# Kernel optimization log

Hardware: AMD Instinct MI355X
Metric: run time of the kernel (lower is better)

The kernel has to match this reference:

```python
import jax, jax.numpy as jnp
import numpy as np
import math

DIM = 256
B, H, W = 8, 64, 64


def setup_inputs() -> dict:
    key = jax.random.key(0)
    ks = jax.random.split(key, 8)
    d4 = DIM // 4
    s = 1.0 / math.sqrt(DIM)
    return {
        "sem": jax.random.normal(ks[0], (B, DIM, H, W), jnp.float32),
        "foren": jax.random.normal(ks[1], (B, DIM, H, W), jnp.float32),
        "Wq": jax.random.normal(ks[2], (d4, DIM), jnp.float32) * s,
        "bq": jnp.zeros((d4,), jnp.float32),
        "Wk": jax.random.normal(ks[3], (d4, DIM), jnp.float32) * s,
        "bk": jnp.zeros((d4,), jnp.float32),
        "Wv": jax.random.normal(ks[4], (DIM, DIM), jnp.float32) * s,
        "bv": jnp.zeros((DIM,), jnp.float32),
        "gamma": jnp.zeros((1,), jnp.float32),
    }


def reference(sem, foren, Wq, bq, Wk, bk, Wv, bv, gamma):
    Bn, C, Hn, Wn = sem.shape
    HW = Hn * Wn
    # 1x1 convs == per-pixel linear projections
    q = jnp.einsum('oc,bchw->bohw', Wq, sem) + bq[None, :, None, None]
    k = jnp.einsum('oc,bchw->bohw', Wk, foren) + bk[None, :, None, None]
    v = jnp.einsum('oc,bchw->bohw', Wv, foren) + bv[None, :, None, None]
    q = q.reshape(Bn, -1, HW).transpose(0, 2, 1)        # [B, HW, C/4]
    k = k.reshape(Bn, -1, HW)                           # [B, C/4, HW]
    v = v.reshape(Bn, C, HW)                            # [B, C, HW]
    attn = jnp.einsum('bnd,bdm->bnm', q, k) / math.sqrt(C // 4)
    attn = jax.nn.softmax(attn, axis=-1)                # [B, HW, HW]
    out = jnp.einsum('bcm,bnm->bcn', v, attn).reshape(Bn, C, Hn, Wn)
    return sem + gamma * out
```

## Files before the change

kernel.cpp:

```cpp
#include <hip/hip_runtime.h>
#include <stdint.h>

typedef unsigned short u16;
typedef unsigned int u32;
typedef short s16x8 __attribute__((ext_vector_type(8)));
typedef float f32x4 __attribute__((ext_vector_type(4)));
typedef float f32x16 __attribute__((ext_vector_type(16)));
typedef u32 u32x2 __attribute__((ext_vector_type(2)));

#define DIM 256
#define HW  4096
#define NB  8
#define QSCL 0.18033688011112042f

template <int N> struct ic { static constexpr int value = N; };

__device__ __forceinline__ u16 f2bf(float f) {
  union { float f; unsigned u; } v; v.f = f;
  unsigned r = v.u + 0x7FFFu + ((v.u >> 16) & 1u);
  return (u16)(r >> 16);
}
__device__ __forceinline__ float fexp2(float x) { return __builtin_amdgcn_exp2f(x); }

typedef __attribute__((address_space(1))) const void gvoid_c;
typedef __attribute__((address_space(3))) void lvoid;
__device__ __forceinline__ void gload_lds16(const void* g, void* l) {
  __builtin_amdgcn_global_load_lds((gvoid_c*)g, (lvoid*)l, 16, 0, 0);
}
__device__ __forceinline__ f32x16 mfma32(s16x8 a, s16x8 b, f32x16 c) {
  return __builtin_amdgcn_mfma_f32_32x32x16_bf16(a, b, c, 0, 0, 0);
}
__device__ __forceinline__ f32x4 mfma16(s16x8 a, s16x8 b, f32x4 c) {
  return __builtin_amdgcn_mfma_f32_16x16x32_bf16(a, b, c, 0, 0, 0);
}

__global__ void prep_w(const float* __restrict__ Wq, const float* __restrict__ Wk,
                       const float* __restrict__ Wv, u16* __restrict__ dst,
                       u32* __restrict__ knmax_u) {
  int idx = blockIdx.x * 256 + threadIdx.x;
  if (blockIdx.x == 0 && threadIdx.x < 8) knmax_u[threadIdx.x] = 0u;
  float v;
  if (idx < 16384)        v = Wq[idx] * QSCL;
  else if (idx < 32768)   v = Wk[idx - 16384];
  else                    v = Wv[idx - 32768];
  dst[idx] = f2bf(v);
}

__global__ __launch_bounds__(256) void proj_all(
    const float* __restrict__ sem, const float* __restrict__ foren,
    const u16* __restrict__ Wqb, const u16* __restrict__ Wkb, const u16* __restrict__ Wvb,
    const float* __restrict__ bq, const float* __restrict__ bk, const float* __restrict__ bv,
    u16* __restrict__ Qo, u16* __restrict__ Ko, u16* __restrict__ Vo,
    float* __restrict__ qnsq, u32* __restrict__ knmax_u) {
  __shared__ u16 lds[16384];
  const bool qpath = blockIdx.x < 512;
  const int bid = qpath ? blockIdx.x : blockIdx.x - 512;
  const int t = threadIdx.x, b = bid & 7, n0 = (bid >> 3) * 64;
  const float* X = qpath ? sem : foren;
  {
    const int px = t & 63, cb = (t >> 6) * 8, swz = (px & 31) * 8;
    for (int i = 0; i < 8; ++i) {
      int c0 = i * 32 + cb;
      size_t gb = ((size_t)b * DIM + c0) * HW + n0 + px;
      s16x8 us;
#pragma unroll
      for (int j = 0; j < 8; ++j) us[j] = (short)f2bf(X[gb + (size_t)j * HW]);
      *(s16x8*)(lds + px * 256 + (c0 ^ swz)) = us;
    }
  }
  __syncthreads();
  const int w = t >> 6, lane = t & 63, l15 = lane & 15, g = lane >> 4;

  if (qpath) {
    const int px = w * 16 + l15;
    s16x8 bx[8];
#pragma unroll
    for (int kc = 0; kc < 8; ++kc)
      bx[kc] = *(const s16x8*)(lds + px * 256 + (((kc * 4 + g) ^ (px & 31)) * 8));
    float nrm = 0.f;
#pragma unroll
    for (int ct = 0; ct < 4; ++ct) {
      f32x4 bb = *(const f32x4*)(bq + ct * 16 + 4 * g);
      f32x4 acc;
#pragma unroll
      for (int j = 0; j < 4; ++j) acc[j] = bb[j] * QSCL;
#pragma unroll
      for (int kc = 0; kc < 8; ++kc) {
        s16x8 aw = *(const s16x8*)(Wqb + (ct * 16 + l15) * 256 + kc * 32 + g * 8);
        acc = mfma16(aw, bx[kc], acc);
      }
      u32 lo = (u32)f2bf(acc[0]) | ((u32)f2bf(acc[1]) << 16);
      u32 hi = (u32)f2bf(acc[2]) | ((u32)f2bf(acc[3]) << 16);
      u32x2 pk; pk[0] = lo; pk[1] = hi;
      *(u32x2*)(Qo + ((size_t)b * HW + n0 + px) * 64 + ct * 16 + 4 * g) = pk;
#pragma unroll
      for (int j = 0; j < 4; ++j) nrm += acc[j] * acc[j];
    }
    nrm += __shfl_xor(nrm, 16);
    nrm += __shfl_xor(nrm, 32);
    if (g == 0) qnsq[(size_t)b * HW + n0 + px] = nrm;
    return;
  }
  {
    const int px = w * 16 + l15;
    s16x8 bx[8];
#pragma unroll
    for (int kc = 0; kc < 8; ++kc)
      bx[kc] = *(const s16x8*)(lds + px * 256 + (((kc * 4 + g) ^ (px & 31)) * 8));
    float nrm = 0.f;
#pragma unroll
    for (int ct = 0; ct < 4; ++ct) {
      f32x4 acc = *(const f32x4*)(bk + ct * 16 + 4 * g);
#pragma unroll
      for (int kc = 0; kc < 8; ++kc) {
        s16x8 aw = *(const s16x8*)(Wkb + (ct * 16 + l15) * 256 + kc * 32 + g * 8);
        acc = mfma16(aw, bx[kc], acc);
      }
      u32 lo = (u32)f2bf(acc[0]) | ((u32)f2bf(acc[1]) << 16);
      u32 hi = (u32)f2bf(acc[2]) | ((u32)f2bf(acc[3]) << 16);
      u32x2 pk; pk[0] = lo; pk[1] = hi;
      *(u32x2*)(Ko + ((size_t)b * HW + n0 + px) * 64 + ct * 16 + 4 * g) = pk;
#pragma unroll
      for (int j = 0; j < 4; ++j) nrm += acc[j] * acc[j];
    }
    nrm += __shfl_xor(nrm, 16);
    nrm += __shfl_xor(nrm, 32);
    nrm = fmaxf(nrm, __shfl_xor(nrm, 1));
    nrm = fmaxf(nrm, __shfl_xor(nrm, 2));
    nrm = fmaxf(nrm, __shfl_xor(nrm, 4));
    nrm = fmaxf(nrm, __shfl_xor(nrm, 8));
    if (lane == 0) atomicMax(knmax_u + b, __float_as_uint(nrm));
  }
#pragma unroll
  for (int ct2 = 0; ct2 < 4; ++ct2) {
    const int c0 = w * 64 + ct2 * 16;
    s16x8 aw[8];
#pragma unroll
    for (int kc = 0; kc < 8; ++kc)
      aw[kc] = *(const s16x8*)(Wvb + (c0 + l15) * 256 + kc * 32 + g * 8);
#pragma unroll
    for (int pxt = 0; pxt < 4; ++pxt) {
      const int px = pxt * 16 + l15;
      f32x4 acc = *(const f32x4*)(bv + c0 + 4 * g);
#pragma unroll
      for (int kc = 0; kc < 8; ++kc) {
        s16x8 bxp = *(const s16x8*)(lds + px * 256 + (((kc * 4 + g) ^ (px & 31)) * 8));
        acc = mfma16(aw[kc], bxp, acc);
      }
#pragma unroll
      for (int j = 0; j < 4; ++j)
        Vo[((size_t)b * DIM + c0 + 4 * g + j) * HW + n0 + pxt * 16 + l15] = f2bf(acc[j]);
    }
  }
}

__global__ __launch_bounds__(1024, 4) void attn4(
    const u16* __restrict__ Qg, const u16* __restrict__ Kg, const u16* __restrict__ Vg,
    const float* __restrict__ qnsq, const u32* __restrict__ knmax_u,
    const float* __restrict__ sem, const float* __restrict__ gamma_p,
    float* __restrict__ out) {
  __shared__ u16 lds[33280];
  char* ldsb = (char*)lds;
  const int t = threadIdx.x;
  const int b = blockIdx.x & 7;
  const int n0 = (blockIdx.x >> 3) << 7;
  const int w = t >> 6, lane = t & 63;
  const int l31 = lane & 31, g5 = lane >> 5;
  const bool qk = w < 8;

  const u16* Qb = Qg + (size_t)b * HW * 64;
  const u16* Kb = Kg + (size_t)b * HW * 64;
  const u16* Vb = Vg + (size_t)b * DIM * HW;

  const int hh = w >> 2, rr = w & 3;
  const int key0 = hh * 32 + l31;
  const int qrow = rr * 32 + l31;
  int ka[4], pw_[4];
  s16x8 qb[4];
  float mr = 0.f, lreg = 0.f;
  if (qk) {
#pragma unroll
    for (int ks = 0; ks < 4; ++ks) {
      ka[ks] = key0 * 128 + (((ks * 2 + g5) ^ (key0 & 7)) * 16);
      qb[ks] = *(const s16x8*)(Qb + (size_t)(n0 + qrow) * 64 + ks * 16 + g5 * 8);
    }
#pragma unroll
    for (int jg = 0; jg < 4; ++jg)
      pw_[jg] = 49152 + qrow * 128 + (((hh * 4 + jg) ^ (qrow & 7)) * 16) + g5 * 8;
    mr = sqrtf(qnsq[(size_t)b * HW + n0 + qrow] * __uint_as_float(knmax_u[b])) * 1.02f;
  }

  const int w8 = w - 8;
  const int srow = lane >> 3;
  const int sx = ((lane & 7) ^ srow) * 8;

  const int rb = w & 3, cb2 = (w >> 2) & 3;
  int pa[4], va[2][4];
#pragma unroll
  for (int ks = 0; ks < 4; ++ks) {
    int r = rb * 32 + l31;
    pa[ks] = 49152 + r * 128 + (((ks * 2 + g5) ^ (r & 7)) * 16);
#pragma unroll
    for (int ct = 0; ct < 2; ++ct) {
      int c = cb2 * 64 + ct * 32 + l31;
      va[ct][ks] = 16384 + c * 128 + (((ks * 2 + g5) ^ (c & 7)) * 16);
    }
  }
  f32x16 O[2] = {};

  auto tile = [&](auto KB, int kt) {
    constexpr int KBUF = decltype(KB)::value;
    if (qk) {
      f32x16 sc = {};
#pragma unroll
      for (int ks = 0; ks < 4; ++ks) {
        s16x8 ak = *(const s16x8*)(ldsb + ka[ks] + KBUF * 8192);
        sc = mfma32(ak, qb[ks], sc);
      }
#pragma unroll
      for (int jg = 0; jg < 4; ++jg) {
        float p0 = fexp2(sc[jg * 4 + 0] - mr);
        float p1 = fexp2(sc[jg * 4 + 1] - mr);
        float p2 = fexp2(sc[jg * 4 + 2] - mr);
        float p3 = fexp2(sc[jg * 4 + 3] - mr);
        lreg += (p0 + p1) + (p2 + p3);
        u32 w0, w1;
        asm("v_cvt_pk_bf16_f32 %0, %1, %2" : "=v"(w0) : "v"(p0), "v"(p1));
        asm("v_cvt_pk_bf16_f32 %0, %1, %2" : "=v"(w1) : "v"(p2), "v"(p3));
        u32x2 pk; pk[0] = w0; pk[1] = w1;
        *(u32x2*)(ldsb + pw_[jg]) = pk;
      }
      asm volatile("s_waitcnt lgkmcnt(0)" ::: "memory");
    } else {
#pragma unroll
      for (int i = 0; i < 4; ++i) {
        int chunk = i * 8 + w8;
        const u16* vsrc = Vb + (size_t)(chunk * 8 + srow) * HW + kt * 64 + sx;
        gload_lds16(vsrc, (void*)(lds + 8192 + chunk * 512));
      }
      {
        const u16* ksrc = Kb + ((size_t)((kt + 1) * 64 + w8 * 8 + srow)) * 64 + sx;
        gload_lds16(ksrc, (void*)(lds + (KBUF ^ 1) * 4096 + w8 * 512));
      }
      asm volatile("s_waitcnt vmcnt(1)" ::: "memory");
    }
    __builtin_amdgcn_s_barrier();
    __builtin_amdgcn_sched_barrier(0);
    __builtin_amdgcn_s_setprio(1);
#pragma unroll
    for (int ks = 0; ks < 4; ++ks) {
      s16x8 ap = *(const s16x8*)(ldsb + pa[ks]);
      s16x8 v0 = *(const s16x8*)(ldsb + va[0][ks]);
      s16x8 v1 = *(const s16x8*)(ldsb + va[1][ks]);
      O[0] = mfma32(ap, v0, O[0]);
      O[1] = mfma32(ap, v1, O[1]);
    }
    __builtin_amdgcn_s_setprio(0);
    __syncthreads();
  };

  if (!qk) {
    const u16* ksrc = Kb + ((size_t)(w8 * 8 + srow)) * 64 + sx;
    gload_lds16(ksrc, (void*)(lds + w8 * 512));
  }
  __syncthreads();
  for (int kt = 0; kt < 64; kt += 2) {
    tile(ic<0>{}, kt);
    tile(ic<1>{}, kt + 1);
  }

  float* lfp = (float*)(ldsb + 65536);
  if (qk) {
    float ls = lreg + __shfl_xor(lreg, 32);
    if (lane < 32) lfp[hh * 128 + qrow] = ls;
  }
  __syncthreads();
  const float gm = gamma_p[0];
#pragma unroll
  for (int jg = 0; jg < 4; ++jg) {
    const int noff = rb * 32 + jg * 8 + 4 * g5;
    f32x4 l0 = *(const f32x4*)(lfp + noff);
    f32x4 l1 = *(const f32x4*)(lfp + 128 + noff);
    f32x4 inv;
#pragma unroll
    for (int j = 0; j < 4; ++j) inv[j] = __builtin_amdgcn_rcpf(l0[j] + l1[j]);
#pragma unroll
    for (int ct = 0; ct < 2; ++ct) {
      const int c = cb2 * 64 + ct * 32 + l31;
      size_t base = ((size_t)b * DIM + c) * HW + n0 + noff;
      f32x4 sv = *(const f32x4*)(sem + base);
      f32x4 ov;
#pragma unroll
      for (int j = 0; j < 4; ++j)
        ov[j] = sv[j] + gm * (O[ct][jg * 4 + j] * inv[j]);
      *(f32x4*)(out + base) = ov;
    }
  }
}

extern "C" void kernel_launch(void* const* d_in, const int* in_sizes, int n_in,
                              void* d_out, int out_size, void* d_ws, size_t ws_size,
                              hipStream_t stream) {
  const float* sem   = (const float*)d_in[0];
  const float* foren = (const float*)d_in[1];
  const float* Wq    = (const float*)d_in[2];
  const float* bq    = (const float*)d_in[3];
  const float* Wk    = (const float*)d_in[4];
  const float* bk    = (const float*)d_in[5];
  const float* Wv    = (const float*)d_in[6];
  const float* bv    = (const float*)d_in[7];
  const float* gamma = (const float*)d_in[8];
  float* out = (float*)d_out;

  u16* Wqb = (u16*)d_ws;
  u16* Wkb = Wqb + 16384;
  u16* Wvb = Wkb + 16384;
  u16* Q   = Wvb + 65536;
  u16* K   = Q + (size_t)NB * HW * 64;
  u16* V   = K + (size_t)NB * HW * 64;
  float* qnsq = (float*)(V + (size_t)NB * DIM * HW);
  u32* knmax_u = (u32*)(qnsq + (size_t)NB * HW);

  prep_w  <<<384, 256, 0, stream>>>(Wq, Wk, Wv, Wqb, knmax_u);
  proj_all<<<1024, 256, 0, stream>>>(sem, foren, Wqb, Wkb, Wvb, bq, bk, bv, Q, K, V, qnsq, knmax_u);
  attn4   <<<256, 1024, 0, stream>>>(Q, K, V, qnsq, knmax_u, sem, gamma, out);
}
```

Before: 172.3 us.

## Keep softmax probabilities in registers via permlane swap, drop warp specialization

Replaces the warp-specialized attention kernel with attn5, which uses 512 threads in which every wave does both the QK scores and the PV product. The probability tile no longer goes through LDS. It is packed to bf16 and rearranged with permlane32_swap so it can feed the PV MFMA as the B operand directly. K and V tiles are double-buffered with direct global-to-LDS loads issued by all waves. The two key halves are combined through an LDS reduction in the epilogue. This targets LDS round-trips and barrier stalls between producer and consumer waves, at the cost of more accumulator registers per wave (64 floats of O) and fewer waves for hiding latency.

```diff
diff --git a/kernel.cpp b/kernel.cpp
--- a/kernel.cpp
+++ b/kernel.cpp
@@ -21,6 +21,9 @@
   return (u16)(r >> 16);
 }
 __device__ __forceinline__ float fexp2(float x) { return __builtin_amdgcn_exp2f(x); }
+__device__ __forceinline__ u32 cvtpk(float a, float b) {
+  u32 r; asm("v_cvt_pk_bf16_f32 %0, %1, %2" : "=v"(r) : "v"(a), "v"(b)); return r;
+}
 
 typedef __attribute__((address_space(1))) const void gvoid_c;
 typedef __attribute__((address_space(3))) void lvoid;
@@ -154,146 +157,167 @@
   }
 }
 
-__global__ __launch_bounds__(1024, 4) void attn4(
+__global__ __launch_bounds__(512, 2) void attn5(
     const u16* __restrict__ Qg, const u16* __restrict__ Kg, const u16* __restrict__ Vg,
     const float* __restrict__ qnsq, const u32* __restrict__ knmax_u,
     const float* __restrict__ sem, const float* __restrict__ gamma_p,
     float* __restrict__ out) {
-  __shared__ u16 lds[33280];
+  __shared__ u16 lds[40960];
   char* ldsb = (char*)lds;
   const int t = threadIdx.x;
   const int b = blockIdx.x & 7;
   const int n0 = (blockIdx.x >> 3) << 7;
   const int w = t >> 6, lane = t & 63;
   const int l31 = lane & 31, g5 = lane >> 5;
-  const bool qk = w < 8;
+  const int qg = w >> 2, hh = (w >> 1) & 1, cg = w & 1;
 
   const u16* Qb = Qg + (size_t)b * HW * 64;
   const u16* Kb = Kg + (size_t)b * HW * 64;
   const u16* Vb = Vg + (size_t)b * DIM * HW;
 
-  const int hh = w >> 2, rr = w & 3;
-  const int key0 = hh * 32 + l31;
-  const int qrow = rr * 32 + l31;
-  int ka[4], pw_[4];
-  s16x8 qb[4];
-  float mr = 0.f, lreg = 0.f;
-  if (qk) {
-#pragma unroll
-    for (int ks = 0; ks < 4; ++ks) {
-      ka[ks] = key0 * 128 + (((ks * 2 + g5) ^ (key0 & 7)) * 16);
-      qb[ks] = *(const s16x8*)(Qb + (size_t)(n0 + qrow) * 64 + ks * 16 + g5 * 8);
-    }
-#pragma unroll
-    for (int jg = 0; jg < 4; ++jg)
-      pw_[jg] = 49152 + qrow * 128 + (((hh * 4 + jg) ^ (qrow & 7)) * 16) + g5 * 8;
-    mr = sqrtf(qnsq[(size_t)b * HW + n0 + qrow] * __uint_as_float(knmax_u[b])) * 1.02f;
-  }
-
-  const int w8 = w - 8;
+  const int key = hh * 32 + l31;
+  int ka[4];
+#pragma unroll
+  for (int ks = 0; ks < 4; ++ks)
+    ka[ks] = key * 128 + (((ks * 2 + g5) ^ (key & 7)) * 16);
+  s16x8 qb0[4], qb1[4];
+#pragma unroll
+  for (int ks = 0; ks < 4; ++ks) {
+    qb0[ks] = *(const s16x8*)(Qb + (size_t)(n0 + qg * 64 + l31) * 64 + ks * 16 + g5 * 8);
+    qb1[ks] = *(const s16x8*)(Qb + (size_t)(n0 + qg * 64 + 32 + l31) * 64 + ks * 16 + g5 * 8);
+  }
+  const float knsq = __uint_as_float(knmax_u[b]);
+  const float mneg0 = -(sqrtf(qnsq[(size_t)b * HW + n0 + qg * 64 + l31] * knsq) * 1.02f);
+  const float mneg1 = -(sqrtf(qnsq[(size_t)b * HW + n0 + qg * 64 + 32 + l31] * knsq) * 1.02f);
+
+  int va[4][2];
+#pragma unroll
+  for (int cb = 0; cb < 4; ++cb) {
+    int c = cg * 128 + cb * 32 + l31;
+#pragma unroll
+    for (int s = 0; s < 2; ++s)
+      va[cb][s] = c * 128 + (((hh * 4 + s * 2 + g5) ^ (c & 7)) * 16);
+  }
+  f32x16 O[4][2] = {};
+  float lr0 = 0.f, lr1 = 0.f;
+
   const int srow = lane >> 3;
   const int sx = ((lane & 7) ^ srow) * 8;
-
-  const int rb = w & 3, cb2 = (w >> 2) & 3;
-  int pa[4], va[2][4];
-#pragma unroll
-  for (int ks = 0; ks < 4; ++ks) {
-    int r = rb * 32 + l31;
-    pa[ks] = 49152 + r * 128 + (((ks * 2 + g5) ^ (r & 7)) * 16);
-#pragma unroll
-    for (int ct = 0; ct < 2; ++ct) {
-      int c = cb2 * 64 + ct * 32 + l31;
-      va[ct][ks] = 16384 + c * 128 + (((ks * 2 + g5) ^ (c & 7)) * 16);
-    }
-  }
-  f32x16 O[2] = {};
-
-  auto tile = [&](auto KB, int kt) {
-    constexpr int KBUF = decltype(KB)::value;
-    if (qk) {
-      f32x16 sc = {};
-#pragma unroll
-      for (int ks = 0; ks < 4; ++ks) {
-        s16x8 ak = *(const s16x8*)(ldsb + ka[ks] + KBUF * 8192);
-        sc = mfma32(ak, qb[ks], sc);
-      }
-#pragma unroll
-      for (int jg = 0; jg < 4; ++jg) {
-        float p0 = fexp2(sc[jg * 4 + 0] - mr);
-        float p1 = fexp2(sc[jg * 4 + 1] - mr);
-        float p2 = fexp2(sc[jg * 4 + 2] - mr);
-        float p3 = fexp2(sc[jg * 4 + 3] - mr);
-        lreg += (p0 + p1) + (p2 + p3);
-        u32 w0, w1;
-        asm("v_cvt_pk_bf16_f32 %0, %1, %2" : "=v"(w0) : "v"(p0), "v"(p1));
-        asm("v_cvt_pk_bf16_f32 %0, %1, %2" : "=v"(w1) : "v"(p2), "v"(p3));
-        u32x2 pk; pk[0] = w0; pk[1] = w1;
-        *(u32x2*)(ldsb + pw_[jg]) = pk;
-      }
-      asm volatile("s_waitcnt lgkmcnt(0)" ::: "memory");
-    } else {
-#pragma unroll
-      for (int i = 0; i < 4; ++i) {
-        int chunk = i * 8 + w8;
-        const u16* vsrc = Vb + (size_t)(chunk * 8 + srow) * HW + kt * 64 + sx;
-        gload_lds16(vsrc, (void*)(lds + 8192 + chunk * 512));
-      }
-      {
-        const u16* ksrc = Kb + ((size_t)((kt + 1) * 64 + w8 * 8 + srow)) * 64 + sx;
-        gload_lds16(ksrc, (void*)(lds + (KBUF ^ 1) * 4096 + w8 * 512));
-      }
-      asm volatile("s_waitcnt vmcnt(1)" ::: "memory");
-    }
-    __builtin_amdgcn_s_barrier();
-    __builtin_amdgcn_sched_barrier(0);
-    __builtin_amdgcn_s_setprio(1);
-#pragma unroll
-    for (int ks = 0; ks < 4; ++ks) {
-      s16x8 ap = *(const s16x8*)(ldsb + pa[ks]);
-      s16x8 v0 = *(const s16x8*)(ldsb + va[0][ks]);
-      s16x8 v1 = *(const s16x8*)(ldsb + va[1][ks]);
-      O[0] = mfma32(ap, v0, O[0]);
-      O[1] = mfma32(ap, v1, O[1]);
-    }
-    __builtin_amdgcn_s_setprio(0);
+  const u16* kp  = Kb + (size_t)(w * 8 + srow) * 64 + sx;
+  const u16* vp0 = Vb + (size_t)((0 * 8 + w) * 8 + srow) * HW + sx;
+  const u16* vp1 = Vb + (size_t)((1 * 8 + w) * 8 + srow) * HW + sx;
+  const u16* vp2 = Vb + (size_t)((2 * 8 + w) * 8 + srow) * HW + sx;
+  const u16* vp3 = Vb + (size_t)((3 * 8 + w) * 8 + srow) * HW + sx;
+
+  auto STAGE = [&](int kdst, int vdst) {
+    gload_lds16(kp,  (void*)(lds + kdst + w * 512));            kp  += 4096;
+    gload_lds16(vp0, (void*)(lds + vdst + (0 * 8 + w) * 512));  vp0 += 64;
+    gload_lds16(vp1, (void*)(lds + vdst + (1 * 8 + w) * 512));  vp1 += 64;
+    gload_lds16(vp2, (void*)(lds + vdst + (2 * 8 + w) * 512));  vp2 += 64;
+    gload_lds16(vp3, (void*)(lds + vdst + (3 * 8 + w) * 512));  vp3 += 64;
+  };
+
+  s16x8 pb0[2], pb1[2];
+
+  auto tile = [&](auto BUFC, bool dostage) {
+    constexpr int BUF = decltype(BUFC)::value;
+    if (dostage) STAGE((BUF ^ 1) * 4096, 8192 + (BUF ^ 1) * 16384);
+    s16x8 kf[4];
+#pragma unroll
+    for (int ks = 0; ks < 4; ++ks)
+      kf[ks] = *(const s16x8*)(ldsb + BUF * 8192 + ka[ks]);
+#pragma unroll
+    for (int qh = 0; qh < 2; ++qh) {
+      const float mneg = qh == 0 ? mneg0 : mneg1;
+      f32x16 sc;
+#pragma unroll
+      for (int r = 0; r < 16; ++r) sc[r] = mneg;
+#pragma unroll
+      for (int ks = 0; ks < 4; ++ks)
+        sc = mfma32(kf[ks], qh == 0 ? qb0[ks] : qb1[ks], sc);
+      float p[16];
+#pragma unroll
+      for (int r = 0; r < 16; ++r) p[r] = fexp2(sc[r]);
+      float rs = ((p[0] + p[1]) + (p[2] + p[3])) + ((p[4] + p[5]) + (p[6] + p[7])) +
+                 ((p[8] + p[9]) + (p[10] + p[11])) + ((p[12] + p[13]) + (p[14] + p[15]));
+      if (qh == 0) lr0 += rs; else lr1 += rs;
+#pragma unroll
+      for (int s = 0; s < 2; ++s) {
+        u32 x1 = cvtpk(p[s * 8 + 0], p[s * 8 + 1]);
+        u32 x2 = cvtpk(p[s * 8 + 2], p[s * 8 + 3]);
+        u32 y1 = cvtpk(p[s * 8 + 4], p[s * 8 + 5]);
+        u32 y2 = cvtpk(p[s * 8 + 6], p[s * 8 + 7]);
+        u32x2 r1 = __builtin_amdgcn_permlane32_swap(x1, y1, false, false);
+        u32x2 r2 = __builtin_amdgcn_permlane32_swap(x2, y2, false, false);
+        union { u32 wv[4]; s16x8 v; } u;
+        u.wv[0] = r1[0]; u.wv[1] = r2[0]; u.wv[2] = r1[1]; u.wv[3] = r2[1];
+        if (qh == 0) pb0[s] = u.v; else pb1[s] = u.v;
+      }
+    }
+#pragma unroll
+    for (int cb = 0; cb < 4; ++cb) {
+      s16x8 v0 = *(const s16x8*)(ldsb + 16384 + BUF * 32768 + va[cb][0]);
+      s16x8 v1 = *(const s16x8*)(ldsb + 16384 + BUF * 32768 + va[cb][1]);
+      O[cb][0] = mfma32(v0, pb0[0], O[cb][0]);
+      O[cb][0] = mfma32(v1, pb0[1], O[cb][0]);
+      O[cb][1] = mfma32(v0, pb1[0], O[cb][1]);
+      O[cb][1] = mfma32(v1, pb1[1], O[cb][1]);
+    }
     __syncthreads();
   };
 
-  if (!qk) {
-    const u16* ksrc = Kb + ((size_t)(w8 * 8 + srow)) * 64 + sx;
-    gload_lds16(ksrc, (void*)(lds + w8 * 512));
-  }
+  STAGE(0, 8192);
   __syncthreads();
   for (int kt = 0; kt < 64; kt += 2) {
-    tile(ic<0>{}, kt);
-    tile(ic<1>{}, kt + 1);
-  }
-
+    tile(ic<0>{}, true);
+    tile(ic<1>{}, kt + 2 < 64);
+  }
+
+  float ls0 = lr0 + __shfl_xor(lr0, 32);
+  float ls1 = lr1 + __shfl_xor(lr1, 32);
   float* lfp = (float*)(ldsb + 65536);
-  if (qk) {
-    float ls = lreg + __shfl_xor(lreg, 32);
-    if (lane < 32) lfp[hh * 128 + qrow] = ls;
-  }
-  __syncthreads();
+  if (cg == 0 && lane < 32) {
+    lfp[hh * 128 + qg * 64 + l31] = ls0;
+    lfp[hh * 128 + qg * 64 + 32 + l31] = ls1;
+  }
+  const int mb = (qg * 2 + cg) * 16384;
   const float gm = gamma_p[0];
 #pragma unroll
-  for (int jg = 0; jg < 4; ++jg) {
-    const int noff = rb * 32 + jg * 8 + 4 * g5;
-    f32x4 l0 = *(const f32x4*)(lfp + noff);
-    f32x4 l1 = *(const f32x4*)(lfp + 128 + noff);
-    f32x4 inv;
-#pragma unroll
-    for (int j = 0; j < 4; ++j) inv[j] = __builtin_amdgcn_rcpf(l0[j] + l1[j]);
-#pragma unroll
-    for (int ct = 0; ct < 2; ++ct) {
-      const int c = cb2 * 64 + ct * 32 + l31;
-      size_t base = ((size_t)b * DIM + c) * HW + n0 + noff;
-      f32x4 sv = *(const f32x4*)(sem + base);
-      f32x4 ov;
-#pragma unroll
-      for (int j = 0; j < 4; ++j)
-        ov[j] = sv[j] + gm * (O[ct][jg * 4 + j] * inv[j]);
-      *(f32x4*)(out + base) = ov;
+  for (int r = 0; r < 2; ++r) {
+    __syncthreads();
+    if (hh != r) {
+#pragma unroll
+      for (int cb = 0; cb < 4; ++cb) {
+#pragma unroll
+        for (int qd = 0; qd < 4; ++qd) {
+          f32x4 tq;
+          tq[0] = O[cb][r][qd * 4 + 0]; tq[1] = O[cb][r][qd * 4 + 1];
+          tq[2] = O[cb][r][qd * 4 + 2]; tq[3] = O[cb][r][qd * 4 + 3];
+          *(f32x4*)(ldsb + mb + cb * 4096 + l31 * 128 + ((((qd << 1) | g5) ^ (l31 & 7)) * 16)) = tq;
+        }
+      }
+    }
+    __syncthreads();
+    if (hh == r) {
+      float ltot = (r == 0 ? ls0 : ls1) + lfp[(1 - r) * 128 + qg * 64 + r * 32 + l31];
+      float gi = gm * __builtin_amdgcn_rcpf(ltot);
+      const int n = n0 + qg * 64 + r * 32 + l31;
+#pragma unroll
+      for (int cb = 0; cb < 4; ++cb) {
+        f32x16 o = O[cb][r];
+#pragma unroll
+        for (int qd = 0; qd < 4; ++qd) {
+          f32x4 part = *(const f32x4*)(ldsb + mb + cb * 4096 + l31 * 128 + ((((qd << 1) | g5) ^ (l31 & 7)) * 16));
+          o[qd * 4 + 0] += part[0]; o[qd * 4 + 1] += part[1];
+          o[qd * 4 + 2] += part[2]; o[qd * 4 + 3] += part[3];
+        }
+#pragma unroll
+        for (int rg = 0; rg < 16; ++rg) {
+          int c = cg * 128 + cb * 32 + (rg & 3) + 8 * (rg >> 2) + 4 * g5;
+          size_t idx = ((size_t)b * DIM + c) * HW + n;
+          out[idx] = sem[idx] + gi * o[rg];
+        }
+      }
     }
   }
 }
@@ -323,5 +347,5 @@
 
   prep_w  <<<384, 256, 0, stream>>>(Wq, Wk, Wv, Wqb, knmax_u);
   proj_all<<<1024, 256, 0, stream>>>(sem, foren, Wqb, Wkb, Wvb, bq, bk, bv, Q, K, V, qnsq, knmax_u);
-  attn4   <<<256, 1024, 0, stream>>>(Q, K, V, qnsq, knmax_u, sem, gamma, out);
-}
+  attn5   <<<256, 512, 0, stream>>>(Q, K, V, qnsq, knmax_u, sem, gamma, out);
+}
```

Measured after the change: 312.6 us. +81.5%, slower.
